# Optimization experiments

Hardware: AMD Instinct MI355X
Metric: run time of the kernel (lower is better)

The kernel has to match this reference:

```python
import jax, jax.numpy as jnp
import numpy as np

V, D, H, B, T = 4096, 1024, 1024, 64, 512


def setup_inputs() -> dict:
    key = jax.random.key(0)
    k_in, k_emb, k_wc, k_bc, k_wh, k_bh = jax.random.split(key, 6)
    inv_c = 1.0 / np.sqrt(D + H)  # torch Linear init scale ~ U(-1/sqrt(fan_in), ...)
    inv_h = 1.0 / np.sqrt(H)
    return {
        "input": jax.random.randint(k_in, (B, T), 0, V),
        "embed": jax.random.normal(k_emb, (V, D), jnp.float32),       # nn.Embedding weight ~ N(0,1)
        "Wc": jax.random.uniform(k_wc, (D + H, H), jnp.float32, -inv_c, inv_c),  # cell linear (in, out)
        "bc": jax.random.uniform(k_bc, (H,), jnp.float32, -inv_c, inv_c),
        "h0": jnp.zeros((1, H), jnp.float32),                          # init_state parameter
        "Wh": jax.random.uniform(k_wh, (H, V), jnp.float32, -inv_h, inv_h),      # lm_head (in, out)
        "bh": jax.random.uniform(k_bh, (V,), jnp.float32, -inv_h, inv_h),
    }


def reference(input, embed, Wc, bc, h0, Wh, bh):
    d = embed.shape[1]
    x = embed[input]                         # [B, T, D]
    Wx, Wr = Wc[:d], Wc[d:]                  # split concat-linear into input/recurrent parts
    # precompute input projection for all steps (math-equivalent to per-step concat+linear)
    xp = jnp.einsum("btd,dh->bth", x, Wx) + bc   # [B, T, H]
    h_init = jnp.broadcast_to(h0, (x.shape[0], Wr.shape[1]))

    def step(h, xt):
        h_new = jnp.tanh(xt + h @ Wr)
        return h_new, h_new

    _, hs = jax.lax.scan(step, h_init, jnp.swapaxes(xp, 0, 1))  # hs: [T, B, H]
    hs = jnp.swapaxes(hs, 0, 1)              # [B, T, H]
    return hs @ Wh + bh                      # [B, T, V]
```

## Files before the change

kernel.cpp:

```cpp
#include <hip/hip_runtime.h>
#include <hip/hip_bf16.h>
#include <hip/hip_cooperative_groups.h>
#include <cstddef>

typedef short bf16x8 __attribute__((ext_vector_type(8)));
typedef float f32x4 __attribute__((ext_vector_type(4)));


__device__ __forceinline__ short bf16rne(float f) {
  unsigned u = __builtin_bit_cast(unsigned, f);
  u += 0x7fffu + ((u >> 16) & 1u);
  return (short)(u >> 16);
}

__device__ __forceinline__ float fast_tanh(float x) {
  float e = __builtin_amdgcn_exp2f(x * 2.88539008177792681f);
  return 1.0f - 2.0f * __builtin_amdgcn_rcpf(e + 1.0f);
}

__global__ void conv_f32_bf16_x4(const float* __restrict__ src, short* __restrict__ dst, int n4) {
  int i = blockIdx.x * blockDim.x + threadIdx.x;
  if (i >= n4) return;
  float4 v = ((const float4*)src)[i];
  unsigned long long o =
      (unsigned long long)(unsigned short)bf16rne(v.x) |
      ((unsigned long long)(unsigned short)bf16rne(v.y) << 16) |
      ((unsigned long long)(unsigned short)bf16rne(v.z) << 32) |
      ((unsigned long long)(unsigned short)bf16rne(v.w) << 48);
  ((unsigned long long*)dst)[i] = o;
}

__global__ void transpose_conv(const float* __restrict__ src, short* __restrict__ dst,
                               int R, int C) {
  __shared__ float tile[32][33];
  int tx = threadIdx.x, ty = threadIdx.y;
  int bx = blockIdx.x, by = blockIdx.y;
#pragma unroll
  for (int i = 0; i < 4; ++i)
    tile[ty + i * 8][tx] = src[(size_t)(by * 32 + ty + i * 8) * C + bx * 32 + tx];
  __syncthreads();
#pragma unroll
  for (int i = 0; i < 4; ++i)
    dst[(size_t)(bx * 32 + ty + i * 8) * R + by * 32 + tx] = bf16rne(tile[tx][ty + i * 8]);
}

template <bool GATHER, bool OUT_BF16>
__global__ __launch_bounds__(256) void gemm_bf16(
    const short* __restrict__ Abase, const int* __restrict__ gidx,
    const short* __restrict__ BT, const float* __restrict__ bias,
    void* __restrict__ Cout, int M, int N, int K) {
  __shared__ short As[128][40];
  __shared__ short Bs[128][40];
  const int tid = threadIdx.x;
  const int lane = tid & 63;
  const int wave = tid >> 6;
  const int mbase = blockIdx.x * 128;
  const int nbase = blockIdx.y * 128;
  const int wr = (wave >> 1) * 64;
  const int wc = (wave & 1) * 64;
  const int l15 = lane & 15;
  const int lk8 = (lane >> 4) * 8;
  const int r0 = tid >> 2;
  const int kc = (tid & 3) * 8;

  f32x4 acc[4][4] = {};

  for (int k0 = 0; k0 < K; k0 += 32) {
#pragma unroll
    for (int h = 0; h < 2; ++h) {
      int r = r0 + h * 64;
      size_t arow;
      if (GATHER) arow = (size_t)gidx[mbase + r];
      else        arow = (size_t)(mbase + r);
      *(bf16x8*)&As[r][kc] = *(const bf16x8*)(Abase + arow * (size_t)K + k0 + kc);
      *(bf16x8*)&Bs[r][kc] = *(const bf16x8*)(BT + (size_t)(nbase + r) * K + k0 + kc);
    }
    __syncthreads();
    bf16x8 af[4], bfr[4];
#pragma unroll
    for (int i = 0; i < 4; ++i) {
      af[i]  = *(const bf16x8*)&As[wr + i * 16 + l15][lk8];
      bfr[i] = *(const bf16x8*)&Bs[wc + i * 16 + l15][lk8];
    }
#pragma unroll
    for (int i = 0; i < 4; ++i)
#pragma unroll
      for (int j = 0; j < 4; ++j)
        acc[i][j] = __builtin_amdgcn_mfma_f32_16x16x32_bf16(af[i], bfr[j], acc[i][j], 0, 0, 0);
    __syncthreads();
  }

#pragma unroll
  for (int i = 0; i < 4; ++i)
#pragma unroll
    for (int j = 0; j < 4; ++j) {
      int col = nbase + wc + j * 16 + l15;
      float bv = bias ? bias[col] : 0.f;
#pragma unroll
      for (int r = 0; r < 4; ++r) {
        int row = mbase + wr + i * 16 + (lane >> 4) * 4 + r;
        float v = acc[i][j][r] + bv;
        if (OUT_BF16) ((short*)Cout)[(size_t)row * N + col] = bf16rne(v);
        else          ((float*)Cout)[(size_t)row * N + col] = v;
      }
    }
}

__global__ __launch_bounds__(256, 1) void rnn_recur(
    const float* __restrict__ xp, const short* __restrict__ WrT,
    const float* __restrict__ h0, short* __restrict__ hs,
    unsigned int* __restrict__ bar) {
  const int tid = threadIdx.x;
  const int lane = tid & 63;
  const int wave = tid >> 6;
  const int bid = blockIdx.x;
  const int rg = bid >> 4;
  const int rowbase = rg * 16;
  const int colbase = (bid & 15) * 64 + wave * 16;
  const int l15 = lane & 15;
  const int lk8 = (lane >> 4) * 8;
  unsigned int* cnt = bar + rg * 256;

  const int acol = colbase + l15;
  bf16x8 wfrag[32];
#pragma unroll
  for (int ks = 0; ks < 32; ++ks)
    wfrag[ks] = *(const volatile bf16x8*)(WrT + (size_t)acol * 1024 + ks * 32 + lk8);

  const int ob = rowbase + l15;
  const int oc = colbase + (lane >> 4) * 4;

  {
    f32x4 a0 = {}, a1 = {}, a2 = {}, a3 = {};
#pragma unroll
    for (int ks = 0; ks < 32; ks += 4) {
      bf16x8 a[4];
#pragma unroll
      for (int q = 0; q < 4; ++q) {
        const float* hp = h0 + (ks + q) * 32 + lk8;
#pragma unroll
        for (int j = 0; j < 8; ++j) a[q][j] = bf16rne(hp[j]);
      }
      a0 = __builtin_amdgcn_mfma_f32_16x16x32_bf16(wfrag[ks + 0], a[0], a0, 0, 0, 0);
      a1 = __builtin_amdgcn_mfma_f32_16x16x32_bf16(wfrag[ks + 1], a[1], a1, 0, 0, 0);
      a2 = __builtin_amdgcn_mfma_f32_16x16x32_bf16(wfrag[ks + 2], a[2], a2, 0, 0, 0);
      a3 = __builtin_amdgcn_mfma_f32_16x16x32_bf16(wfrag[ks + 3], a[3], a3, 0, 0, 0);
    }
    f32x4 acc = (a0 + a1) + (a2 + a3);
    float4 x4 = *(const float4*)(xp + ((size_t)ob * 512 + 0) * 1024 + oc);
    unsigned long long p =
        (unsigned long long)(unsigned short)bf16rne(fast_tanh(acc[0] + x4.x)) |
        ((unsigned long long)(unsigned short)bf16rne(fast_tanh(acc[1] + x4.y)) << 16) |
        ((unsigned long long)(unsigned short)bf16rne(fast_tanh(acc[2] + x4.z)) << 32) |
        ((unsigned long long)(unsigned short)bf16rne(fast_tanh(acc[3] + x4.w)) << 48);
    __hip_atomic_store((unsigned long long*)(hs + ((size_t)ob * 512 + 0) * 1024 + oc),
                       p, __ATOMIC_RELAXED, __HIP_MEMORY_SCOPE_AGENT);
  }

  float4 xv = *(const float4*)(xp + ((size_t)ob * 512 + 1) * 1024 + oc);

  for (int t = 1; t < 512; ++t) {
    asm volatile("s_waitcnt vmcnt(0)" ::: "memory");
    __builtin_amdgcn_s_barrier();
    if (tid == 0) atomicAdd(cnt, 1u);

    const int tn = (t + 1 < 512) ? (t + 1) : 511;
    float4 xn = *(const float4*)(xp + ((size_t)ob * 512 + tn) * 1024 + oc);

    if (wave == 0) {
      const unsigned target = 16u * (unsigned)t;
      while (__hip_atomic_load(cnt, __ATOMIC_RELAXED, __HIP_MEMORY_SCOPE_AGENT) < target)
        __builtin_amdgcn_s_sleep(1);
    }
    __builtin_amdgcn_s_barrier();
    asm volatile("" ::: "memory");
    __builtin_amdgcn_sched_barrier(0);

    f32x4 a0 = {}, a1 = {}, a2 = {}, a3 = {};
    const short* hrow = hs + ((size_t)(rowbase + l15) * 512 + (t - 1)) * 1024 + lk8;
#pragma unroll
    for (int ks = 0; ks < 32; ks += 4) {
      bf16x8 a[4];
#pragma unroll
      for (int q = 0; q < 4; ++q)
        a[q] = *(const bf16x8*)(hrow + (ks + q) * 32);
      a0 = __builtin_amdgcn_mfma_f32_16x16x32_bf16(wfrag[ks + 0], a[0], a0, 0, 0, 0);
      a1 = __builtin_amdgcn_mfma_f32_16x16x32_bf16(wfrag[ks + 1], a[1], a1, 0, 0, 0);
      a2 = __builtin_amdgcn_mfma_f32_16x16x32_bf16(wfrag[ks + 2], a[2], a2, 0, 0, 0);
      a3 = __builtin_amdgcn_mfma_f32_16x16x32_bf16(wfrag[ks + 3], a[3], a3, 0, 0, 0);
    }
    f32x4 acc = (a0 + a1) + (a2 + a3);

    unsigned long long p =
        (unsigned long long)(unsigned short)bf16rne(fast_tanh(acc[0] + xv.x)) |
        ((unsigned long long)(unsigned short)bf16rne(fast_tanh(acc[1] + xv.y)) << 16) |
        ((unsigned long long)(unsigned short)bf16rne(fast_tanh(acc[2] + xv.z)) << 32) |
        ((unsigned long long)(unsigned short)bf16rne(fast_tanh(acc[3] + xv.w)) << 48);
    __hip_atomic_store((unsigned long long*)(hs + ((size_t)ob * 512 + t) * 1024 + oc),
                       p, __ATOMIC_RELAXED, __HIP_MEMORY_SCOPE_AGENT);
    xv = xn;
  }
}

extern "C" void kernel_launch(void* const* d_in, const int* in_sizes, int n_in,
                              void* d_out, int out_size, void* d_ws, size_t ws_size,
                              hipStream_t stream) {
  const int*   input = (const int*)d_in[0];
  const float* embed = (const float*)d_in[1];
  const float* Wc    = (const float*)d_in[2];
  const float* bc    = (const float*)d_in[3];
  const float* h0    = (const float*)d_in[4];
  const float* Wh    = (const float*)d_in[5];
  const float* bh    = (const float*)d_in[6];

  char* ws = (char*)d_ws;
  float* xp   = (float*)(ws + 0);
  short* hs   = (short*)(ws + 134217728);
  short* embB = (short*)(ws + 201326592);
  short* WxT  = (short*)(ws + 209715200);
  short* WrT  = (short*)(ws + 211812352);
  short* WhT  = (short*)(ws + 213909504);
  unsigned int* bar = (unsigned int*)(ws + 222298112);

  hipMemsetAsync(bar, 0, 4096, stream);

  conv_f32_bf16_x4<<<4096, 256, 0, stream>>>(embed, embB, 1048576);
  transpose_conv<<<dim3(32, 32),  dim3(32, 8), 0, stream>>>(Wc,                WxT, 1024, 1024);
  transpose_conv<<<dim3(32, 32),  dim3(32, 8), 0, stream>>>(Wc + 1024 * 1024,  WrT, 1024, 1024);
  transpose_conv<<<dim3(128, 32), dim3(32, 8), 0, stream>>>(Wh,                WhT, 1024, 4096);

  gemm_bf16<true, false><<<dim3(256, 8), 256, 0, stream>>>(
      embB, input, WxT, bc, (void*)xp, 32768, 1024, 1024);

  {
    const float* xp_c = xp;
    const short* WrT_c = WrT;
    const float* h0_c = h0;
    short* hs_c = hs;
    unsigned int* bar_c = bar;
    void* args[] = {(void*)&xp_c, (void*)&WrT_c, (void*)&h0_c, (void*)&hs_c, (void*)&bar_c};
    hipLaunchCooperativeKernel((const void*)rnn_recur, dim3(64), dim3(256), args, 0, stream);
  }

  gemm_bf16<false, false><<<dim3(256, 32), 256, 0, stream>>>(
      hs, nullptr, WhT, bh, d_out, 32768, 4096, 1024);
}
```

Baseline: 3.308 ms.

## Split recurrence into 8-row groups over 128 blocks with per-wave XCD-local barrier counters

The recurrent kernel now launches 128 blocks, each covering 8 batch rows instead of 16, so the MFMA tiles are half-used (lanes 8-15 duplicate rows and do not store). Each wave signals its own arrival on two counters: a local one incremented with a non-coherent atomic and polled through cache-level loads, and a device-scope one used as a fallback. The block-wide barrier before signalling is removed. The aim is to cut per-step synchronisation latency by keeping polling near the cache close to the blocks, which are assumed to share a chiplet (grouped by bid&7). This relies on the hardware mapping blocks to chiplets round-robin and on the fallback counter for correctness. Doubling the block count also doubles the MFMA work per output row.

```diff
diff --git a/kernel.cpp b/kernel.cpp
--- a/kernel.cpp
+++ b/kernel.cpp
@@ -16,6 +16,17 @@
 __device__ __forceinline__ float fast_tanh(float x) {
   float e = __builtin_amdgcn_exp2f(x * 2.88539008177792681f);
   return 1.0f - 2.0f * __builtin_amdgcn_rcpf(e + 1.0f);
+}
+
+__device__ __forceinline__ unsigned load_l2(const unsigned int* p) {
+  unsigned v;
+  asm volatile("global_load_dword %0, %1, off sc0\n\ts_waitcnt vmcnt(0)"
+               : "=v"(v) : "v"(p) : "memory");
+  return v;
+}
+
+__device__ __forceinline__ void atom_add_l2(unsigned int* p, unsigned v) {
+  asm volatile("global_atomic_add %0, %1, off" :: "v"(p), "v"(v) : "memory");
 }
 
 __global__ void conv_f32_bf16_x4(const float* __restrict__ src, short* __restrict__ dst, int n4) {
@@ -114,12 +125,14 @@
   const int lane = tid & 63;
   const int wave = tid >> 6;
   const int bid = blockIdx.x;
-  const int rg = bid >> 4;
-  const int rowbase = rg * 16;
-  const int colbase = (bid & 15) * 64 + wave * 16;
+  const int d = bid & 7;
+  const int m = bid >> 3;
+  const int rowbase = d * 8;
+  const int colbase = m * 64 + wave * 16;
   const int l15 = lane & 15;
   const int lk8 = (lane >> 4) * 8;
-  unsigned int* cnt = bar + rg * 256;
+  unsigned int* cntL = bar + d * 32;
+  unsigned int* cntG = bar + 512 + d * 32;
 
   const int acol = colbase + l15;
   bf16x8 wfrag[32];
@@ -127,8 +140,9 @@
   for (int ks = 0; ks < 32; ++ks)
     wfrag[ks] = *(const volatile bf16x8*)(WrT + (size_t)acol * 1024 + ks * 32 + lk8);
 
-  const int ob = rowbase + l15;
+  const int bl = rowbase + (l15 & 7);
   const int oc = colbase + (lane >> 4) * 4;
+  const bool do_store = (l15 < 8);
 
   {
     f32x4 a0 = {}, a1 = {}, a2 = {}, a3 = {};
@@ -139,7 +153,7 @@
       for (int q = 0; q < 4; ++q) {
         const float* hp = h0 + (ks + q) * 32 + lk8;
 #pragma unroll
-        for (int j = 0; j < 8; ++j) a[q][j] = bf16rne(hp[j]);
+        for (int jj = 0; jj < 8; ++jj) a[q][jj] = bf16rne(hp[jj]);
       }
       a0 = __builtin_amdgcn_mfma_f32_16x16x32_bf16(wfrag[ks + 0], a[0], a0, 0, 0, 0);
       a1 = __builtin_amdgcn_mfma_f32_16x16x32_bf16(wfrag[ks + 1], a[1], a1, 0, 0, 0);
@@ -147,37 +161,54 @@
       a3 = __builtin_amdgcn_mfma_f32_16x16x32_bf16(wfrag[ks + 3], a[3], a3, 0, 0, 0);
     }
     f32x4 acc = (a0 + a1) + (a2 + a3);
-    float4 x4 = *(const float4*)(xp + ((size_t)ob * 512 + 0) * 1024 + oc);
-    unsigned long long p =
-        (unsigned long long)(unsigned short)bf16rne(fast_tanh(acc[0] + x4.x)) |
-        ((unsigned long long)(unsigned short)bf16rne(fast_tanh(acc[1] + x4.y)) << 16) |
-        ((unsigned long long)(unsigned short)bf16rne(fast_tanh(acc[2] + x4.z)) << 32) |
-        ((unsigned long long)(unsigned short)bf16rne(fast_tanh(acc[3] + x4.w)) << 48);
-    __hip_atomic_store((unsigned long long*)(hs + ((size_t)ob * 512 + 0) * 1024 + oc),
-                       p, __ATOMIC_RELAXED, __HIP_MEMORY_SCOPE_AGENT);
-  }
-
-  float4 xv = *(const float4*)(xp + ((size_t)ob * 512 + 1) * 1024 + oc);
+    if (do_store) {
+      float4 x4 = *(const float4*)(xp + ((size_t)bl * 512 + 0) * 1024 + oc);
+      unsigned long long p =
+          (unsigned long long)(unsigned short)bf16rne(fast_tanh(acc[0] + x4.x)) |
+          ((unsigned long long)(unsigned short)bf16rne(fast_tanh(acc[1] + x4.y)) << 16) |
+          ((unsigned long long)(unsigned short)bf16rne(fast_tanh(acc[2] + x4.z)) << 32) |
+          ((unsigned long long)(unsigned short)bf16rne(fast_tanh(acc[3] + x4.w)) << 48);
+      __hip_atomic_store((unsigned long long*)(hs + ((size_t)bl * 512 + 0) * 1024 + oc),
+                         p, __ATOMIC_RELAXED, __HIP_MEMORY_SCOPE_AGENT);
+    }
+  }
+
+  float4 xv = {0.f, 0.f, 0.f, 0.f};
+  if (do_store)
+    xv = *(const float4*)(xp + ((size_t)bl * 512 + 1) * 1024 + oc);
 
   for (int t = 1; t < 512; ++t) {
     asm volatile("s_waitcnt vmcnt(0)" ::: "memory");
-    __builtin_amdgcn_s_barrier();
-    if (tid == 0) atomicAdd(cnt, 1u);
+    if (lane == 0) {
+      atom_add_l2(cntL, 1u);
+      atomicAdd(cntG, 1u);
+    }
 
     const int tn = (t + 1 < 512) ? (t + 1) : 511;
-    float4 xn = *(const float4*)(xp + ((size_t)ob * 512 + tn) * 1024 + oc);
+    float4 xn = {0.f, 0.f, 0.f, 0.f};
+    if (do_store)
+      xn = *(const float4*)(xp + ((size_t)bl * 512 + tn) * 1024 + oc);
 
     if (wave == 0) {
-      const unsigned target = 16u * (unsigned)t;
-      while (__hip_atomic_load(cnt, __ATOMIC_RELAXED, __HIP_MEMORY_SCOPE_AGENT) < target)
-        __builtin_amdgcn_s_sleep(1);
+      const unsigned target = 64u * (unsigned)t;
+      for (;;) {
+        bool ok = false;
+#pragma unroll 1
+        for (int k = 0; k < 8; ++k) {
+          if (load_l2(cntL) >= target) { ok = true; break; }
+          __builtin_amdgcn_s_sleep(1);
+        }
+        if (ok) break;
+        if (__hip_atomic_load(cntG, __ATOMIC_RELAXED, __HIP_MEMORY_SCOPE_AGENT) >= target)
+          break;
+      }
     }
     __builtin_amdgcn_s_barrier();
     asm volatile("" ::: "memory");
     __builtin_amdgcn_sched_barrier(0);
 
     f32x4 a0 = {}, a1 = {}, a2 = {}, a3 = {};
-    const short* hrow = hs + ((size_t)(rowbase + l15) * 512 + (t - 1)) * 1024 + lk8;
+    const short* hrow = hs + ((size_t)bl * 512 + (t - 1)) * 1024 + lk8;
 #pragma unroll
     for (int ks = 0; ks < 32; ks += 4) {
       bf16x8 a[4];
@@ -191,13 +222,15 @@
     }
     f32x4 acc = (a0 + a1) + (a2 + a3);
 
-    unsigned long long p =
-        (unsigned long long)(unsigned short)bf16rne(fast_tanh(acc[0] + xv.x)) |
-        ((unsigned long long)(unsigned short)bf16rne(fast_tanh(acc[1] + xv.y)) << 16) |
-        ((unsigned long long)(unsigned short)bf16rne(fast_tanh(acc[2] + xv.z)) << 32) |
-        ((unsigned long long)(unsigned short)bf16rne(fast_tanh(acc[3] + xv.w)) << 48);
-    __hip_atomic_store((unsigned long long*)(hs + ((size_t)ob * 512 + t) * 1024 + oc),
-                       p, __ATOMIC_RELAXED, __HIP_MEMORY_SCOPE_AGENT);
+    if (do_store) {
+      unsigned long long p =
+          (unsigned long long)(unsigned short)bf16rne(fast_tanh(acc[0] + xv.x)) |
+          ((unsigned long long)(unsigned short)bf16rne(fast_tanh(acc[1] + xv.y)) << 16) |
+          ((unsigned long long)(unsigned short)bf16rne(fast_tanh(acc[2] + xv.z)) << 32) |
+          ((unsigned long long)(unsigned short)bf16rne(fast_tanh(acc[3] + xv.w)) << 48);
+      __hip_atomic_store((unsigned long long*)(hs + ((size_t)bl * 512 + t) * 1024 + oc),
+                         p, __ATOMIC_RELAXED, __HIP_MEMORY_SCOPE_AGENT);
+    }
     xv = xn;
   }
 }
@@ -239,7 +272,7 @@
     short* hs_c = hs;
     unsigned int* bar_c = bar;
     void* args[] = {(void*)&xp_c, (void*)&WrT_c, (void*)&h0_c, (void*)&hs_c, (void*)&bar_c};
-    hipLaunchCooperativeKernel((const void*)rnn_recur, dim3(64), dim3(256), args, 0, stream);
+    hipLaunchCooperativeKernel((const void*)rnn_recur, dim3(128), dim3(256), args, 0, stream);
   }
 
   gemm_bf16<false, false><<<dim3(256, 32), 256, 0, stream>>>(
```

New measurement: 4.762 ms. 43.9% more time.

## Replace per-step atomic counter barrier with per-wave flags polled via ballot

Applied to the files above, without the earlier changes.

The recurrence kernel's per-step synchronization changes from a block barrier plus an atomic counter per row group to per-wave, per-timestep flags in global memory. Each wave publishes a flag after storing its slice of h_t, and each wave polls all 64 flags of its row group with a cache-bypassing load and a ballot. This removes the intra-block s_barriers and the serialized atomicAdd, so waves can proceed independently and latency per step drops. It needs a larger flag array memset each launch and more polling traffic.

```diff
diff --git a/kernel.cpp b/kernel.cpp
--- a/kernel.cpp
+++ b/kernel.cpp
@@ -16,6 +16,13 @@
 __device__ __forceinline__ float fast_tanh(float x) {
   float e = __builtin_amdgcn_exp2f(x * 2.88539008177792681f);
   return 1.0f - 2.0f * __builtin_amdgcn_rcpf(e + 1.0f);
+}
+
+__device__ __forceinline__ unsigned load_if(const unsigned int* p) {
+  unsigned v;
+  asm volatile("global_load_dword %0, %1, off sc0 sc1\n\ts_waitcnt vmcnt(0)"
+               : "=v"(v) : "v"(p) : "memory");
+  return v;
 }
 
 __global__ void conv_f32_bf16_x4(const float* __restrict__ src, short* __restrict__ dst, int n4) {
@@ -109,17 +116,18 @@
 __global__ __launch_bounds__(256, 1) void rnn_recur(
     const float* __restrict__ xp, const short* __restrict__ WrT,
     const float* __restrict__ h0, short* __restrict__ hs,
-    unsigned int* __restrict__ bar) {
+    unsigned int* __restrict__ flags) {
   const int tid = threadIdx.x;
   const int lane = tid & 63;
   const int wave = tid >> 6;
   const int bid = blockIdx.x;
   const int rg = bid >> 4;
+  const int m = bid & 15;
   const int rowbase = rg * 16;
-  const int colbase = (bid & 15) * 64 + wave * 16;
+  const int colbase = m * 64 + wave * 16;
   const int l15 = lane & 15;
   const int lk8 = (lane >> 4) * 8;
-  unsigned int* cnt = bar + rg * 256;
+  const int own_idx = m * 4 + wave;
 
   const int acol = colbase + l15;
   bf16x8 wfrag[32];
@@ -139,7 +147,7 @@
       for (int q = 0; q < 4; ++q) {
         const float* hp = h0 + (ks + q) * 32 + lk8;
 #pragma unroll
-        for (int j = 0; j < 8; ++j) a[q][j] = bf16rne(hp[j]);
+        for (int jj = 0; jj < 8; ++jj) a[q][jj] = bf16rne(hp[jj]);
       }
       a0 = __builtin_amdgcn_mfma_f32_16x16x32_bf16(wfrag[ks + 0], a[0], a0, 0, 0, 0);
       a1 = __builtin_amdgcn_mfma_f32_16x16x32_bf16(wfrag[ks + 1], a[1], a1, 0, 0, 0);
@@ -155,29 +163,32 @@
         ((unsigned long long)(unsigned short)bf16rne(fast_tanh(acc[3] + x4.w)) << 48);
     __hip_atomic_store((unsigned long long*)(hs + ((size_t)ob * 512 + 0) * 1024 + oc),
                        p, __ATOMIC_RELAXED, __HIP_MEMORY_SCOPE_AGENT);
+    asm volatile("s_waitcnt vmcnt(0)" ::: "memory");
+    if (lane == 0)
+      __hip_atomic_store(&flags[(size_t)(0 * 4 + rg) * 64 + own_idx], 1u,
+                         __ATOMIC_RELAXED, __HIP_MEMORY_SCOPE_AGENT);
   }
 
   float4 xv = *(const float4*)(xp + ((size_t)ob * 512 + 1) * 1024 + oc);
 
   for (int t = 1; t < 512; ++t) {
-    asm volatile("s_waitcnt vmcnt(0)" ::: "memory");
-    __builtin_amdgcn_s_barrier();
-    if (tid == 0) atomicAdd(cnt, 1u);
-
     const int tn = (t + 1 < 512) ? (t + 1) : 511;
     float4 xn = *(const float4*)(xp + ((size_t)ob * 512 + tn) * 1024 + oc);
 
-    if (wave == 0) {
-      const unsigned target = 16u * (unsigned)t;
-      while (__hip_atomic_load(cnt, __ATOMIC_RELAXED, __HIP_MEMORY_SCOPE_AGENT) < target)
+    {
+      const unsigned int* fb = flags + (size_t)((t - 1) * 4 + rg) * 64;
+      for (;;) {
+        unsigned fv = load_if(fb + lane);
+        bool ok = (fv != 0u) || (lane == own_idx);
+        if (__ballot(ok) == ~0ull) break;
         __builtin_amdgcn_s_sleep(1);
-    }
-    __builtin_amdgcn_s_barrier();
+      }
+    }
     asm volatile("" ::: "memory");
     __builtin_amdgcn_sched_barrier(0);
 
     f32x4 a0 = {}, a1 = {}, a2 = {}, a3 = {};
-    const short* hrow = hs + ((size_t)(rowbase + l15) * 512 + (t - 1)) * 1024 + lk8;
+    const short* hrow = hs + ((size_t)ob * 512 + (t - 1)) * 1024 + lk8;
 #pragma unroll
     for (int ks = 0; ks < 32; ks += 4) {
       bf16x8 a[4];
@@ -198,6 +209,10 @@
         ((unsigned long long)(unsigned short)bf16rne(fast_tanh(acc[3] + xv.w)) << 48);
     __hip_atomic_store((unsigned long long*)(hs + ((size_t)ob * 512 + t) * 1024 + oc),
                        p, __ATOMIC_RELAXED, __HIP_MEMORY_SCOPE_AGENT);
+    asm volatile("s_waitcnt vmcnt(0)" ::: "memory");
+    if (lane == 0)
+      __hip_atomic_store(&flags[(size_t)(t * 4 + rg) * 64 + own_idx], 1u,
+                         __ATOMIC_RELAXED, __HIP_MEMORY_SCOPE_AGENT);
     xv = xn;
   }
 }
@@ -220,9 +235,9 @@
   short* WxT  = (short*)(ws + 209715200);
   short* WrT  = (short*)(ws + 211812352);
   short* WhT  = (short*)(ws + 213909504);
-  unsigned int* bar = (unsigned int*)(ws + 222298112);
-
-  hipMemsetAsync(bar, 0, 4096, stream);
+  unsigned int* flags = (unsigned int*)(ws + 222298112);
+
+  hipMemsetAsync(flags, 0, 2048 * 64 * 4, stream);
 
   conv_f32_bf16_x4<<<4096, 256, 0, stream>>>(embed, embB, 1048576);
   transpose_conv<<<dim3(32, 32),  dim3(32, 8), 0, stream>>>(Wc,                WxT, 1024, 1024);
@@ -237,8 +252,8 @@
     const short* WrT_c = WrT;
     const float* h0_c = h0;
     short* hs_c = hs;
-    unsigned int* bar_c = bar;
-    void* args[] = {(void*)&xp_c, (void*)&WrT_c, (void*)&h0_c, (void*)&hs_c, (void*)&bar_c};
+    unsigned int* flags_c = flags;
+    void* args[] = {(void*)&xp_c, (void*)&WrT_c, (void*)&h0_c, (void*)&hs_c, (void*)&flags_c};
     hipLaunchCooperativeKernel((const void*)rnn_recur, dim3(64), dim3(256), args, 0, stream);
   }
 
```

Measured after the change: 3.478 ms. 1.05x slower.
